# Performance work log

Hardware: AMD Instinct MI355X
Metric: run time of the kernel (lower is better)

Reference implementation:

```python
import jax, jax.numpy as jnp
import numpy as np


def setup_inputs() -> dict:
    key = jax.random.key(0)
    ks = jax.random.split(key, 8)
    B, C, W, H = 4, 256, 64, 64
    dqk = C // 8
    s_in = 1.0 / np.sqrt(C)
    return {
        "x": jax.random.normal(ks[0], (B, C, W, H), dtype=jnp.float32),
        "Wq": jax.random.normal(ks[1], (dqk, C), dtype=jnp.float32) * s_in,
        "bq": jnp.zeros((dqk,), dtype=jnp.float32),
        "Wk": jax.random.normal(ks[2], (dqk, C), dtype=jnp.float32) * s_in,
        "bk": jnp.zeros((dqk,), dtype=jnp.float32),
        "Wv": jax.random.normal(ks[3], (C, C), dtype=jnp.float32) * s_in,
        "bv": jnp.zeros((C,), dtype=jnp.float32),
        "gamma": jnp.zeros((1,), dtype=jnp.float32),
    }


def reference(x, Wq, bq, Wk, bk, Wv, bv, gamma):
    B, C, W, H = x.shape
    N = W * H
    xf = x.reshape(B, C, N)  # flatten spatial: B x C x N
    # 1x1 convs == per-pixel linear projections over channels
    q = jnp.einsum("bcn,dc->bnd", xf, Wq) + bq            # B x N x dqk
    k = jnp.einsum("bcn,dc->bdn", xf, Wk) + bk[None, :, None]  # B x dqk x N
    v = jnp.einsum("bcn,dc->bdn", xf, Wv) + bv[None, :, None]  # B x C x N
    # unscaled attention, softmax over keys (last dim)
    attn = jax.nn.softmax(jnp.einsum("bnd,bdm->bnm", q, k), axis=-1)  # B x N x N
    # out[b,c,i] = sum_j v[b,c,j] * attn[b,i,j]  (bmm with attn^T)
    out = jnp.einsum("bcj,bij->bci", v, attn).reshape(B, C, W, H)
    return gamma[0] * out + x
```

## Files before the change

### kernel.cpp

```cpp
#include <hip/hip_runtime.h>

#define BB 4
#define CC 256
#define NN 4096

typedef __attribute__((ext_vector_type(8))) short bh8;
typedef __attribute__((ext_vector_type(4))) float f32x4;

#define WPK_OFF  0
#define BALL_OFF 163840
#define QBF_OFF  165888
#define KBF_OFF  (165888 + 1048576)
#define VBF_OFF  (165888 + 2097152)

typedef const __attribute__((address_space(1))) void* gas_t;
typedef __attribute__((address_space(3))) void* las_t;
__device__ inline void gld16(const void* g, void* l) {
    __builtin_amdgcn_global_load_lds((gas_t)g, (las_t)l, 16, 0, 0);
}

__device__ inline int pack2bf(float a, float b) {
    unsigned ua = __builtin_bit_cast(unsigned, a) + 0x8000u;
    unsigned ub = __builtin_bit_cast(unsigned, b) + 0x8000u;
    return (int)__builtin_amdgcn_perm(ub, ua, 0x07060302u);
}
__device__ inline short f2bf1(float a) {
    return (short)((__builtin_bit_cast(unsigned, a) + 0x8000u) >> 16);
}

__global__ __launch_bounds__(256) void prep_w(const float* __restrict__ Wq,
        const float* __restrict__ bq, const float* __restrict__ Wk,
        const float* __restrict__ bk, const float* __restrict__ Wv,
        const float* __restrict__ bv, short* __restrict__ Wpk,
        float* __restrict__ ball) {
    int tid = blockIdx.x * 256 + threadIdx.x;
    if (tid < 10240) {
        int lane = tid & 63;
        int fc = tid >> 6;
        int mt = fc >> 3, ck = fc & 7;
        int m = mt * 16 + (lane & 15);
        int c0 = ck * 32 + (lane >> 4) * 8;
        const float* wrow;
        if (m < 32)      wrow = Wq + m * 256;
        else if (m < 64) wrow = Wk + (m - 32) * 256;
        else             wrow = Wv + (m - 64) * 256;
        int d[4];
        #pragma unroll
        for (int p = 0; p < 4; ++p)
            d[p] = pack2bf(wrow[c0 + 2 * p], wrow[c0 + 2 * p + 1]);
        *(int4*)(Wpk + tid * 8) = make_int4(d[0], d[1], d[2], d[3]);
    }
    if (tid < 320) {
        float b2 = tid < 32 ? bq[tid] : (tid < 64 ? bk[tid - 32] : bv[tid - 64]);
        ball[tid] = b2;
    }
}

__global__ __launch_bounds__(256) void proj(const float* __restrict__ x,
        const short* __restrict__ Wpk, const float* __restrict__ ball,
        short* __restrict__ qbf, short* __restrict__ kbf,
        short* __restrict__ vbf) {
    int t = threadIdx.x;
    int w = t >> 6, lane = t & 63, quad = lane >> 4, c15 = lane & 15;
    int gw = blockIdx.x * 4 + w;
    int tile = gw >> 1, mh = gw & 1;
    int b = tile >> 8, n0 = (tile & 255) * 16;
    const float* xb = x + (size_t)b * CC * NN;

    bh8 af[8];
    #pragma unroll
    for (int ck = 0; ck < 8; ++ck) {
        float v[8];
        #pragma unroll
        for (int e = 0; e < 8; ++e)
            v[e] = xb[(size_t)(ck * 32 + quad * 8 + e) * NN + n0 + c15];
        int d[4];
        #pragma unroll
        for (int p = 0; p < 4; ++p) d[p] = pack2bf(v[2 * p], v[2 * p + 1]);
        af[ck] = __builtin_bit_cast(bh8, make_int4(d[0], d[1], d[2], d[3]));
    }

    #pragma unroll
    for (int mpi = 0; mpi < 5; ++mpi) {
        int mp = mh * 5 + mpi;
        int mtA = mp * 2, mtB = mp * 2 + 1;
        float blA = ball[mtA * 16 + c15], blB = ball[mtB * 16 + c15];
        f32x4 accA = {blA, blA, blA, blA}, accB = {blB, blB, blB, blB};
        #pragma unroll
        for (int ck = 0; ck < 8; ++ck) {
            bh8 wfA = *(const bh8*)(Wpk + ((mtA * 8 + ck) * 64 + lane) * 8);
            bh8 wfB = *(const bh8*)(Wpk + ((mtB * 8 + ck) * 64 + lane) * 8);
            accA = __builtin_amdgcn_mfma_f32_16x16x32_bf16(af[ck], wfA, accA, 0, 0, 0);
            accB = __builtin_amdgcn_mfma_f32_16x16x32_bf16(af[ck], wfB, accB, 0, 0, 0);
        }
        #pragma unroll
        for (int half = 0; half < 2; ++half) {
            int mt = mp * 2 + half;
            f32x4 acc = half ? accB : accA;
            if (mt < 4) {
                short* dst = (mt < 2) ? qbf : kbf;
                int m = (mt & 1) * 16 + c15;
                #pragma unroll
                for (int r = 0; r < 4; ++r)
                    dst[(size_t)(b * NN + n0 + quad * 4 + r) * 32 + m] = f2bf1(acc[r]);
            } else {
                int c = mt * 16 + c15 - 64;
                int2 pk;
                pk.x = pack2bf(acc[0], acc[1]);
                pk.y = pack2bf(acc[2], acc[3]);
                *(int2*)(vbf + (size_t)b * CC * NN + (size_t)c * NN + n0 + quad * 4) = pk;
            }
        }
    }
}

__global__ __launch_bounds__(512, 4) void flash_attn(
        const short* __restrict__ qbf, const short* __restrict__ kbf,
        const short* __restrict__ vbf, const float* __restrict__ x,
        const float* __restrict__ gamma, float* __restrict__ out) {
    __shared__ char lds[81920];

    int bid = blockIdx.x;
    int b = bid & 3, i0 = (bid >> 2) * 64;
    int t = threadIdx.x;
    int w = t >> 6, lane = t & 63, quad = lane >> 4, c15 = lane & 15;
    int mg = w & 3, nh = w >> 2, jsub = w & 3;

    const short* qb = qbf + (size_t)b * NN * 32;
    const short* kb = kbf + (size_t)b * NN * 32;
    const short* vb = vbf + (size_t)b * CC * NN;

    bh8 qf0 = *(const bh8*)(qb + (size_t)(i0 + nh * 32 + c15) * 32 + quad * 8);
    bh8 qf1 = *(const bh8*)(qb + (size_t)(i0 + nh * 32 + 16 + c15) * 32 + quad * 8);

    int vrow = w * 32 + (lane >> 3);
    int glog = (lane & 7) ^ ((lane >> 3) & 7);
    const short* vsg = vb + (size_t)vrow * NN + glog * 8;
    char* vdst = lds + w * 4096;

    const short* kptr = kb + (size_t)(jsub * 16 + c15) * 32 + quad * 8;

    char* Pt = lds + 65536;
    float* lred = (float*)lds;

    f32x4 acc[4][2];
    #pragma unroll
    for (int ms = 0; ms < 4; ++ms) {
        acc[ms][0] = (f32x4){0.f, 0.f, 0.f, 0.f};
        acc[ms][1] = (f32x4){0.f, 0.f, 0.f, 0.f};
    }
    float lsum0 = 0.f, lsum1 = 0.f;
    const f32x4 initc = {-12.f, -12.f, -12.f, -12.f};

    #pragma unroll
    for (int r = 0; r < 4; ++r) gld16(vsg + r * 8 * NN, vdst + r * 1024);
    bh8 kf = *(const bh8*)kptr;
    __syncthreads();

    for (int jt = 0; jt < 64; ++jt) {
        int cur = jt & 1;
        f32x4 sa0 = __builtin_amdgcn_mfma_f32_16x16x32_bf16(kf, qf0, initc, 0, 0, 0);
        f32x4 sa1 = __builtin_amdgcn_mfma_f32_16x16x32_bf16(kf, qf1, initc, 0, 0, 0);
        bh8 kfn = *(const bh8*)(kptr + (size_t)((jt + 1) & 63) * 2048);
        float p0[4], p1[4];
        #pragma unroll
        for (int r = 0; r < 4; ++r) {
            p0[r] = __expf(sa0[r]); lsum0 += p0[r];
            p1[r] = __expf(sa1[r]); lsum1 += p1[r];
        }
        char* Ptc = Pt + cur * 8192;
        int g = jsub * 2 + (quad >> 1);
        int pb0 = (nh * 32 + c15) * 128 + ((g ^ (c15 & 7)) * 16) + (quad & 1) * 8;
        *(int2*)(Ptc + pb0) = make_int2(pack2bf(p0[0], p0[1]), pack2bf(p0[2], p0[3]));
        *(int2*)(Ptc + pb0 + 2048) = make_int2(pack2bf(p1[0], p1[1]), pack2bf(p1[2], p1[3]));

        __syncthreads();

        if (jt < 63) {
            const short* vs = vsg + (jt + 1) * 64;
            char* vd = vdst + ((cur ^ 1) << 15);
            #pragma unroll
            for (int r = 0; r < 4; ++r) gld16(vs + r * 8 * NN, vd + r * 1024);
        }

        const char* Vb = lds + cur * 32768;
        #pragma unroll
        for (int kk = 0; kk < 2; ++kk) {
            int gs = ((kk * 4 + quad) ^ (c15 & 7)) * 16;
            bh8 pfa = *(const bh8*)(Ptc + (nh * 32 + c15) * 128 + gs);
            bh8 pfb = *(const bh8*)(Ptc + (nh * 32 + 16 + c15) * 128 + gs);
            #pragma unroll
            for (int ms = 0; ms < 4; ++ms) {
                int c = mg * 64 + ms * 16 + c15;
                bh8 vf = *(const bh8*)(Vb + c * 128 + gs);
                acc[ms][0] = __builtin_amdgcn_mfma_f32_16x16x32_bf16(vf, pfa, acc[ms][0], 0, 0, 0);
                acc[ms][1] = __builtin_amdgcn_mfma_f32_16x16x32_bf16(vf, pfb, acc[ms][1], 0, 0, 0);
            }
        }
        kf = kfn;
    }

    lsum0 += __shfl_xor(lsum0, 16); lsum0 += __shfl_xor(lsum0, 32);
    lsum1 += __shfl_xor(lsum1, 16); lsum1 += __shfl_xor(lsum1, 32);
    __syncthreads();
    if (lane < 16) {
        lred[w * 32 + lane] = lsum0;
        lred[w * 32 + 16 + lane] = lsum1;
    }
    __syncthreads();
    float l0 = lred[(nh * 4 + 0) * 32 + c15] + lred[(nh * 4 + 1) * 32 + c15]
             + lred[(nh * 4 + 2) * 32 + c15] + lred[(nh * 4 + 3) * 32 + c15];
    float l1 = lred[(nh * 4 + 0) * 32 + 16 + c15] + lred[(nh * 4 + 1) * 32 + 16 + c15]
             + lred[(nh * 4 + 2) * 32 + 16 + c15] + lred[(nh * 4 + 3) * 32 + 16 + c15];
    float linv0 = 1.0f / l0, linv1 = 1.0f / l1;

    float gm = gamma[0];
    const float* xb2 = x + (size_t)b * CC * NN;
    float* ob = out + (size_t)b * CC * NN;
    int ia = i0 + nh * 32 + c15, ib2 = ia + 16;
    #pragma unroll
    for (int ms = 0; ms < 4; ++ms) {
        #pragma unroll
        for (int r = 0; r < 4; ++r) {
            int c = mg * 64 + ms * 16 + quad * 4 + r;
            ob[(size_t)c * NN + ia]  = gm * acc[ms][0][r] * linv0 + xb2[(size_t)c * NN + ia];
            ob[(size_t)c * NN + ib2] = gm * acc[ms][1][r] * linv1 + xb2[(size_t)c * NN + ib2];
        }
    }
}

extern "C" void kernel_launch(void* const* d_in, const int* in_sizes, int n_in,
                              void* d_out, int out_size, void* d_ws, size_t ws_size,
                              hipStream_t stream) {
    const float* x     = (const float*)d_in[0];
    const float* Wq    = (const float*)d_in[1];
    const float* bq    = (const float*)d_in[2];
    const float* Wk    = (const float*)d_in[3];
    const float* bk    = (const float*)d_in[4];
    const float* Wv    = (const float*)d_in[5];
    const float* bv    = (const float*)d_in[6];
    const float* gamma = (const float*)d_in[7];
    float* out = (float*)d_out;
    char*  ws  = (char*)d_ws;
    short* Wpk  = (short*)(ws + WPK_OFF);
    float* ball = (float*)(ws + BALL_OFF);
    short* qbf  = (short*)(ws + QBF_OFF);
    short* kbf  = (short*)(ws + KBF_OFF);
    short* vbf  = (short*)(ws + VBF_OFF);

    prep_w<<<40, 256, 0, stream>>>(Wq, bq, Wk, bk, Wv, bv, Wpk, ball);
    proj<<<512, 256, 0, stream>>>(x, Wpk, ball, qbf, kbf, vbf);
    flash_attn<<<256, 512, 0, stream>>>(qbf, kbf, vbf, x, gamma, out);
}
```

Baseline: 141.6 us.

## Warp-specialize flash attention into producer and consumer waves

Splits the eight waves of each block into four producer waves and four consumer waves. Producers compute QK^T scores, exp, row sums and the bf16 P tile, and issue V prefetch loads one tile ahead. Consumers run only the PV MFMAs, each with a 64-channel by 64-row accumulator tile. The goal is to overlap the softmax/exp work with the PV matrix multiply across waves and to remove per-iteration scoring from the consumers. In exchange the consumer accumulator array doubles, so launch bounds drop from 4 to 2 blocks per SM. Half the waves also do no MFMA work during the PV phase, and both groups still meet at one barrier per tile.

```diff
diff --git a/kernel.cpp b/kernel.cpp
--- a/kernel.cpp
+++ b/kernel.cpp
@@ -114,7 +114,7 @@
     }
 }
 
-__global__ __launch_bounds__(512, 4) void flash_attn(
+__global__ __launch_bounds__(512, 2) void flash_attn(
         const short* __restrict__ qbf, const short* __restrict__ kbf,
         const short* __restrict__ vbf, const float* __restrict__ x,
         const float* __restrict__ gamma, float* __restrict__ out) {
@@ -124,107 +124,137 @@
     int b = bid & 3, i0 = (bid >> 2) * 64;
     int t = threadIdx.x;
     int w = t >> 6, lane = t & 63, quad = lane >> 4, c15 = lane & 15;
-    int mg = w & 3, nh = w >> 2, jsub = w & 3;
+    int pw = w & 3;
+    bool producer = (w < 4);
 
     const short* qb = qbf + (size_t)b * NN * 32;
     const short* kb = kbf + (size_t)b * NN * 32;
     const short* vb = vbf + (size_t)b * CC * NN;
 
-    bh8 qf0 = *(const bh8*)(qb + (size_t)(i0 + nh * 32 + c15) * 32 + quad * 8);
-    bh8 qf1 = *(const bh8*)(qb + (size_t)(i0 + nh * 32 + 16 + c15) * 32 + quad * 8);
-
-    int vrow = w * 32 + (lane >> 3);
-    int glog = (lane & 7) ^ ((lane >> 3) & 7);
-    const short* vsg = vb + (size_t)vrow * NN + glog * 8;
-    char* vdst = lds + w * 4096;
-
-    const short* kptr = kb + (size_t)(jsub * 16 + c15) * 32 + quad * 8;
-
     char* Pt = lds + 65536;
     float* lred = (float*)lds;
 
-    f32x4 acc[4][2];
+    const f32x4 initc = {-12.f, -12.f, -12.f, -12.f};
+
+    bh8 qf[4];
+    bh8 kf;
+    float lsum[4] = {0.f, 0.f, 0.f, 0.f};
+    const short* kptr = kb + (size_t)(pw * 16 + c15) * 32 + quad * 8;
+    int glog = (lane & 7) ^ ((lane >> 3) & 7);
+    const short* vsg = vb + (size_t)(pw * 64 + (lane >> 3)) * NN + glog * 8;
+    int pgs = ((pw * 2 + (quad >> 1)) ^ (c15 & 7)) * 16 + (quad & 1) * 8;
+
+    f32x4 acc[4][4];
     #pragma unroll
-    for (int ms = 0; ms < 4; ++ms) {
-        acc[ms][0] = (f32x4){0.f, 0.f, 0.f, 0.f};
-        acc[ms][1] = (f32x4){0.f, 0.f, 0.f, 0.f};
-    }
-    float lsum0 = 0.f, lsum1 = 0.f;
-    const f32x4 initc = {-12.f, -12.f, -12.f, -12.f};
-
-    #pragma unroll
-    for (int r = 0; r < 4; ++r) gld16(vsg + r * 8 * NN, vdst + r * 1024);
-    bh8 kf = *(const bh8*)kptr;
+    for (int ms = 0; ms < 4; ++ms)
+        #pragma unroll
+        for (int f = 0; f < 4; ++f) acc[ms][f] = (f32x4){0.f, 0.f, 0.f, 0.f};
+
+    if (producer) {
+        #pragma unroll
+        for (int f = 0; f < 4; ++f)
+            qf[f] = *(const bh8*)(qb + (size_t)(i0 + f * 16 + c15) * 32 + quad * 8);
+        kf = *(const bh8*)kptr;
+        {
+            char* vd = lds + pw * 8192;
+            #pragma unroll
+            for (int r = 0; r < 8; ++r) gld16(vsg + r * 8 * NN, vd + r * 1024);
+            f32x4 sa[4];
+            #pragma unroll
+            for (int f = 0; f < 4; ++f)
+                sa[f] = __builtin_amdgcn_mfma_f32_16x16x32_bf16(kf, qf[f], initc, 0, 0, 0);
+            #pragma unroll
+            for (int f = 0; f < 4; ++f) {
+                float p[4];
+                #pragma unroll
+                for (int r = 0; r < 4; ++r) { p[r] = __expf(sa[f][r]); lsum[f] += p[r]; }
+                *(int2*)(Pt + (f * 16 + c15) * 128 + pgs) =
+                    make_int2(pack2bf(p[0], p[1]), pack2bf(p[2], p[3]));
+            }
+        }
+        kf = *(const bh8*)(kptr + 2048);
+    }
     __syncthreads();
 
     for (int jt = 0; jt < 64; ++jt) {
-        int cur = jt & 1;
-        f32x4 sa0 = __builtin_amdgcn_mfma_f32_16x16x32_bf16(kf, qf0, initc, 0, 0, 0);
-        f32x4 sa1 = __builtin_amdgcn_mfma_f32_16x16x32_bf16(kf, qf1, initc, 0, 0, 0);
-        bh8 kfn = *(const bh8*)(kptr + (size_t)((jt + 1) & 63) * 2048);
-        float p0[4], p1[4];
-        #pragma unroll
-        for (int r = 0; r < 4; ++r) {
-            p0[r] = __expf(sa0[r]); lsum0 += p0[r];
-            p1[r] = __expf(sa1[r]); lsum1 += p1[r];
-        }
-        char* Ptc = Pt + cur * 8192;
-        int g = jsub * 2 + (quad >> 1);
-        int pb0 = (nh * 32 + c15) * 128 + ((g ^ (c15 & 7)) * 16) + (quad & 1) * 8;
-        *(int2*)(Ptc + pb0) = make_int2(pack2bf(p0[0], p0[1]), pack2bf(p0[2], p0[3]));
-        *(int2*)(Ptc + pb0 + 2048) = make_int2(pack2bf(p1[0], p1[1]), pack2bf(p1[2], p1[3]));
-
+        if (producer) {
+            if (jt < 63) {
+                int jn = jt + 1;
+                const short* vs = vsg + (size_t)jn * 64;
+                char* vd = lds + (jn & 1) * 32768 + pw * 8192;
+                #pragma unroll
+                for (int r = 0; r < 8; ++r) gld16(vs + r * 8 * NN, vd + r * 1024);
+                bh8 kfn = *(const bh8*)(kptr + (size_t)((jn + 1) & 63) * 2048);
+                f32x4 sa[4];
+                #pragma unroll
+                for (int f = 0; f < 4; ++f)
+                    sa[f] = __builtin_amdgcn_mfma_f32_16x16x32_bf16(kf, qf[f], initc, 0, 0, 0);
+                char* Ptc = Pt + (jn & 1) * 8192;
+                #pragma unroll
+                for (int f = 0; f < 4; ++f) {
+                    float p[4];
+                    #pragma unroll
+                    for (int r = 0; r < 4; ++r) { p[r] = __expf(sa[f][r]); lsum[f] += p[r]; }
+                    *(int2*)(Ptc + (f * 16 + c15) * 128 + pgs) =
+                        make_int2(pack2bf(p[0], p[1]), pack2bf(p[2], p[3]));
+                }
+                kf = kfn;
+            }
+        } else {
+            const char* Vb = lds + (jt & 1) * 32768;
+            const char* Ptc = Pt + (jt & 1) * 8192;
+            #pragma unroll
+            for (int kk = 0; kk < 2; ++kk) {
+                int gs = ((kk * 4 + quad) ^ (c15 & 7)) * 16;
+                bh8 pf[4];
+                #pragma unroll
+                for (int f = 0; f < 4; ++f)
+                    pf[f] = *(const bh8*)(Ptc + (f * 16 + c15) * 128 + gs);
+                #pragma unroll
+                for (int ms = 0; ms < 4; ++ms) {
+                    int c = pw * 64 + ms * 16 + c15;
+                    bh8 vf = *(const bh8*)(Vb + c * 128 + gs);
+                    #pragma unroll
+                    for (int f = 0; f < 4; ++f)
+                        acc[ms][f] = __builtin_amdgcn_mfma_f32_16x16x32_bf16(
+                            vf, pf[f], acc[ms][f], 0, 0, 0);
+                }
+            }
+        }
         __syncthreads();
-
-        if (jt < 63) {
-            const short* vs = vsg + (jt + 1) * 64;
-            char* vd = vdst + ((cur ^ 1) << 15);
-            #pragma unroll
-            for (int r = 0; r < 4; ++r) gld16(vs + r * 8 * NN, vd + r * 1024);
-        }
-
-        const char* Vb = lds + cur * 32768;
-        #pragma unroll
-        for (int kk = 0; kk < 2; ++kk) {
-            int gs = ((kk * 4 + quad) ^ (c15 & 7)) * 16;
-            bh8 pfa = *(const bh8*)(Ptc + (nh * 32 + c15) * 128 + gs);
-            bh8 pfb = *(const bh8*)(Ptc + (nh * 32 + 16 + c15) * 128 + gs);
+    }
+
+    if (producer) {
+        #pragma unroll
+        for (int f = 0; f < 4; ++f) {
+            lsum[f] += __shfl_xor(lsum[f], 16);
+            lsum[f] += __shfl_xor(lsum[f], 32);
+        }
+        if (quad == 0) {
+            #pragma unroll
+            for (int f = 0; f < 4; ++f) lred[pw * 64 + f * 16 + c15] = lsum[f];
+        }
+    }
+    __syncthreads();
+
+    if (!producer) {
+        float gm = gamma[0];
+        const float* xb2 = x + (size_t)b * CC * NN;
+        float* ob = out + (size_t)b * CC * NN;
+        #pragma unroll
+        for (int f = 0; f < 4; ++f) {
+            float linv = 1.0f / (lred[f * 16 + c15] + lred[64 + f * 16 + c15]
+                               + lred[128 + f * 16 + c15] + lred[192 + f * 16 + c15]);
+            int i = i0 + f * 16 + c15;
             #pragma unroll
             for (int ms = 0; ms < 4; ++ms) {
-                int c = mg * 64 + ms * 16 + c15;
-                bh8 vf = *(const bh8*)(Vb + c * 128 + gs);
-                acc[ms][0] = __builtin_amdgcn_mfma_f32_16x16x32_bf16(vf, pfa, acc[ms][0], 0, 0, 0);
-                acc[ms][1] = __builtin_amdgcn_mfma_f32_16x16x32_bf16(vf, pfb, acc[ms][1], 0, 0, 0);
-            }
-        }
-        kf = kfn;
-    }
-
-    lsum0 += __shfl_xor(lsum0, 16); lsum0 += __shfl_xor(lsum0, 32);
-    lsum1 += __shfl_xor(lsum1, 16); lsum1 += __shfl_xor(lsum1, 32);
-    __syncthreads();
-    if (lane < 16) {
-        lred[w * 32 + lane] = lsum0;
-        lred[w * 32 + 16 + lane] = lsum1;
-    }
-    __syncthreads();
-    float l0 = lred[(nh * 4 + 0) * 32 + c15] + lred[(nh * 4 + 1) * 32 + c15]
-             + lred[(nh * 4 + 2) * 32 + c15] + lred[(nh * 4 + 3) * 32 + c15];
-    float l1 = lred[(nh * 4 + 0) * 32 + 16 + c15] + lred[(nh * 4 + 1) * 32 + 16 + c15]
-             + lred[(nh * 4 + 2) * 32 + 16 + c15] + lred[(nh * 4 + 3) * 32 + 16 + c15];
-    float linv0 = 1.0f / l0, linv1 = 1.0f / l1;
-
-    float gm = gamma[0];
-    const float* xb2 = x + (size_t)b * CC * NN;
-    float* ob = out + (size_t)b * CC * NN;
-    int ia = i0 + nh * 32 + c15, ib2 = ia + 16;
-    #pragma unroll
-    for (int ms = 0; ms < 4; ++ms) {
-        #pragma unroll
-        for (int r = 0; r < 4; ++r) {
-            int c = mg * 64 + ms * 16 + quad * 4 + r;
-            ob[(size_t)c * NN + ia]  = gm * acc[ms][0][r] * linv0 + xb2[(size_t)c * NN + ia];
-            ob[(size_t)c * NN + ib2] = gm * acc[ms][1][r] * linv1 + xb2[(size_t)c * NN + ib2];
+                #pragma unroll
+                for (int r = 0; r < 4; ++r) {
+                    int c = pw * 64 + ms * 16 + quad * 4 + r;
+                    ob[(size_t)c * NN + i] = gm * acc[ms][f][r] * linv
+                                           + xb2[(size_t)c * NN + i];
+                }
+            }
         }
     }
 }
```

Result: slower. 152.3 us (+7.6%).
